# Kernel tuning notes

Measured on AMD Instinct MI355X. Metric: run time of the kernel, lower is better.

The kernel has to match this reference:

```python
import jax, jax.numpy as jnp
import numpy as np

B, U, D = 128, 200, 512

def setup_inputs() -> dict:
    key = jax.random.key(0)
    k1, k2, k3 = jax.random.split(key, 3)
    input_real = jax.random.normal(k1, (B, D, D), dtype=jnp.float32)
    input_imag = jax.random.normal(k2, (B, D, D), dtype=jnp.float32)
    # keras 'uniform' initializer: U(-0.05, 0.05); unit_norm constraint normalizes over axes (1,2)
    kernel = jax.random.uniform(k3, (U, D, 2), dtype=jnp.float32, minval=-0.05, maxval=0.05)
    kernel = kernel / jnp.linalg.norm(kernel.reshape(U, -1), axis=1)[:, None, None]
    return {"input_real": input_real, "input_imag": input_imag, "kernel": kernel}

def reference(input_real, input_imag, kernel):
    # kernel: [U, D, 2] -> real/imag measurement vectors
    kr = kernel[:, :, 0]  # [U, D]
    ki = kernel[:, :, 1]  # [U, D]
    # Original: M_real = kr kr^T - ki ki^T ; M_imag = ki kr^T + kr ki^T (outer products per unit)
    # out[b,n] = trace(R_b @ M_real_n) - trace(I_b @ M_imag_n)
    # trace(A @ (u v^T)) = sum_ij A[i,j] u[j] v[i] -> quadratic form, avoids [B,U,D,D] tiles.
    t_real = (jnp.einsum('bij,nj,ni->bn', input_real, kr, kr)
              - jnp.einsum('bij,nj,ni->bn', input_real, ki, ki))
    t_imag = (jnp.einsum('bij,nj,ni->bn', input_imag, ki, kr)
              + jnp.einsum('bij,nj,ni->bn', input_imag, kr, ki))
    return t_real - t_imag  # [B, U]
```

## Files before the change

kernel.cpp:

```cpp
#include <hip/hip_runtime.h>
#include <hip/hip_bf16.h>

#define BB 128
#define UU 200
#define DD 512
#define NPAD 256
#define ASTR 40
#define WSTR 40

typedef __attribute__((ext_vector_type(8))) short short8;
typedef __attribute__((ext_vector_type(4))) float f32x4;

__device__ __forceinline__ unsigned short f2bf(float x) {
    union { float f; unsigned u; } v; v.f = x;
    unsigned r = v.u + 0x7FFFu + ((v.u >> 16) & 1u);
    return (unsigned short)(r >> 16);
}

__global__ void zero_out_kernel(float* __restrict__ out) {
    int i = blockIdx.x * 256 + threadIdx.x;
    if (i < BB * UU) out[i] = 0.0f;
}

__global__ __launch_bounds__(512, 4) void cm_gemm_kernel(
    const float* __restrict__ Ar, const float* __restrict__ Ai,
    const float* __restrict__ Kt, float* __restrict__ out)
{
    __shared__ short sAr[BB * ASTR];
    __shared__ short sAi[BB * ASTR];
    __shared__ short sWr[NPAD * WSTR];
    __shared__ short sWi[NPAD * WSTR];

    const int tid  = threadIdx.x;
    const int irow = blockIdx.x;
    const int w    = tid >> 6;
    const int lane = tid & 63;
    const int mw   = (w & 1) * 64;
    const int nw   = (w >> 1) * 64;
    const int rrow = lane & 15;
    const int quad = lane >> 4;

    const int nW = tid >> 1;
    const int jh = (tid & 1) * 16;
    float krI = 0.0f, kiI = 0.0f;
    if (nW < UU) {
        const float2* k2 = (const float2*)Kt;
        float2 s = k2[(size_t)nW * DD + irow];
        krI = s.x; kiI = s.y;
    }

    const int brow0 = tid >> 3;
    const int grp   = tid & 7;
    const size_t aoff0 = (size_t)brow0 * DD * DD + (size_t)irow * DD + (size_t)grp * 4;
    const size_t aoff1 = aoff0 + (size_t)64 * DD * DD;

    f32x4 acc[4][4];
#pragma unroll
    for (int a = 0; a < 4; ++a)
#pragma unroll
        for (int b = 0; b < 4; ++b) acc[a][b] = (f32x4)(0.0f);

    for (int jw = 0; jw < DD; jw += 32) {
        f32x4 vr0 = *(const f32x4*)(Ar + aoff0 + jw);
        f32x4 vr1 = *(const f32x4*)(Ar + aoff1 + jw);
        f32x4 vi0 = *(const f32x4*)(Ai + aoff0 + jw);
        f32x4 vi1 = *(const f32x4*)(Ai + aoff1 + jw);

        {
            union { unsigned short s[4]; uint2 u; } t0, t1, t2, t3;
#pragma unroll
            for (int q = 0; q < 4; ++q) {
                t0.s[q] = f2bf(vr0[q]); t1.s[q] = f2bf(vr1[q]);
                t2.s[q] = f2bf(vi0[q]); t3.s[q] = f2bf(vi1[q]);
            }
            *(uint2*)&sAr[ brow0       * ASTR + grp * 4] = t0.u;
            *(uint2*)&sAr[(brow0 + 64) * ASTR + grp * 4] = t1.u;
            *(uint2*)&sAi[ brow0       * ASTR + grp * 4] = t2.u;
            *(uint2*)&sAi[(brow0 + 64) * ASTR + grp * 4] = t3.u;
        }

        if (nW < UU) {
            const f32x4* kv = (const f32x4*)(Kt + (size_t)nW * DD * 2 + (size_t)(jw + jh) * 2);
#pragma unroll
            for (int q = 0; q < 8; ++q) {
                f32x4 v = kv[q];
                float wr0 =  krI * v[0] - kiI * v[1];
                float wi0 = -(krI * v[1] + kiI * v[0]);
                float wr1 =  krI * v[2] - kiI * v[3];
                float wi1 = -(krI * v[3] + kiI * v[2]);
                unsigned pr = (unsigned)f2bf(wr0) | ((unsigned)f2bf(wr1) << 16);
                unsigned pi = (unsigned)f2bf(wi0) | ((unsigned)f2bf(wi1) << 16);
                *(unsigned*)&sWr[nW * WSTR + jh + 2 * q] = pr;
                *(unsigned*)&sWi[nW * WSTR + jh + 2 * q] = pi;
            }
        } else {
#pragma unroll
            for (int q = 0; q < 8; ++q) {
                *(unsigned*)&sWr[nW * WSTR + jh + 2 * q] = 0u;
                *(unsigned*)&sWi[nW * WSTR + jh + 2 * q] = 0u;
            }
        }

        __syncthreads();

#pragma unroll
        for (int ph = 0; ph < 2; ++ph) {
            const short* sA = ph ? sAi : sAr;
            const short* sW = ph ? sWi : sWr;
            short8 af[4], bf[4];
#pragma unroll
            for (int t = 0; t < 4; ++t) {
                af[t] = *(const short8*)&sA[(mw + t * 16 + rrow) * ASTR + quad * 8];
                bf[t] = *(const short8*)&sW[(nw + t * 16 + rrow) * WSTR + quad * 8];
            }
#pragma unroll
            for (int ti = 0; ti < 4; ++ti)
#pragma unroll
                for (int tj = 0; tj < 4; ++tj)
                    acc[ti][tj] = __builtin_amdgcn_mfma_f32_16x16x32_bf16(
                        af[ti], bf[tj], acc[ti][tj], 0, 0, 0);
        }

        __syncthreads();
    }

#pragma unroll
    for (int ti = 0; ti < 4; ++ti) {
        int m = mw + ti * 16 + quad * 4;
#pragma unroll
        for (int tj = 0; tj < 4; ++tj) {
            int n = nw + tj * 16 + rrow;
            if (n < UU) {
#pragma unroll
                for (int r = 0; r < 4; ++r)
                    atomicAdd(&out[(size_t)(m + r) * UU + n], acc[ti][tj][r]);
            }
        }
    }
}

extern "C" void kernel_launch(void* const* d_in, const int* in_sizes, int n_in,
                              void* d_out, int out_size, void* d_ws, size_t ws_size,
                              hipStream_t stream) {
    const float* Ar = (const float*)d_in[0];
    const float* Ai = (const float*)d_in[1];
    const float* Kt = (const float*)d_in[2];
    float* out = (float*)d_out;

    hipLaunchKernelGGL(zero_out_kernel, dim3((BB * UU + 255) / 256), dim3(256), 0, stream, out);
    hipLaunchKernelGGL(cm_gemm_kernel, dim3(DD), dim3(512), 0, stream, Ar, Ai, Kt, out);
}
```

Measured before the change: 375.3 us.

## Prefetch next A tile into registers and replace atomics with workspace reduction

The A loads for the next k-step are now issued before the MFMA phase, a register-level software prefetch meant to hide global load latency. When enough workspace is available, each of the 512 blocks writes its partial [B,U] result to its own workspace slice with plain stores. A separate reduce kernel then sums the slices in 8 groups and finishes with fewer atomics. This removes heavy contention from 512-way atomicAdd on the same outputs. The cost is about 52 MB of extra workspace writes and reads plus an added launch.

```diff
diff --git a/kernel.cpp b/kernel.cpp
--- a/kernel.cpp
+++ b/kernel.cpp
@@ -7,6 +7,7 @@
 #define NPAD 256
 #define ASTR 40
 #define WSTR 40
+#define NSPLIT 512
 
 typedef __attribute__((ext_vector_type(8))) short short8;
 typedef __attribute__((ext_vector_type(4))) float f32x4;
@@ -22,9 +23,21 @@
     if (i < BB * UU) out[i] = 0.0f;
 }
 
+__global__ void reduce_kernel(const float* __restrict__ ws, float* __restrict__ out) {
+    int o = blockIdx.x * 256 + threadIdx.x;
+    if (o >= BB * UU) return;
+    int p0 = blockIdx.y * (NSPLIT / 8);
+    float s = 0.0f;
+#pragma unroll 8
+    for (int p = 0; p < NSPLIT / 8; ++p)
+        s += ws[(size_t)(p0 + p) * (BB * UU) + o];
+    atomicAdd(&out[o], s);
+}
+
+template<bool USE_WS>
 __global__ __launch_bounds__(512, 4) void cm_gemm_kernel(
     const float* __restrict__ Ar, const float* __restrict__ Ai,
-    const float* __restrict__ Kt, float* __restrict__ out)
+    const float* __restrict__ Kt, float* __restrict__ dst)
 {
     __shared__ short sAr[BB * ASTR];
     __shared__ short sAi[BB * ASTR];
@@ -60,11 +73,13 @@
 #pragma unroll
         for (int b = 0; b < 4; ++b) acc[a][b] = (f32x4)(0.0f);
 
-    for (int jw = 0; jw < DD; jw += 32) {
-        f32x4 vr0 = *(const f32x4*)(Ar + aoff0 + jw);
-        f32x4 vr1 = *(const f32x4*)(Ar + aoff1 + jw);
-        f32x4 vi0 = *(const f32x4*)(Ai + aoff0 + jw);
-        f32x4 vi1 = *(const f32x4*)(Ai + aoff1 + jw);
+    f32x4 vr0 = *(const f32x4*)(Ar + aoff0);
+    f32x4 vr1 = *(const f32x4*)(Ar + aoff1);
+    f32x4 vi0 = *(const f32x4*)(Ai + aoff0);
+    f32x4 vi1 = *(const f32x4*)(Ai + aoff1);
+
+    for (int it = 0; it < 16; ++it) {
+        const int jw = it * 32;
 
         {
             union { unsigned short s[4]; uint2 u; } t0, t1, t2, t3;
@@ -103,6 +118,12 @@
 
         __syncthreads();
 
+        const int jn = (it < 15) ? (jw + 32) : 0;
+        f32x4 nr0 = *(const f32x4*)(Ar + aoff0 + jn);
+        f32x4 nr1 = *(const f32x4*)(Ar + aoff1 + jn);
+        f32x4 ni0 = *(const f32x4*)(Ai + aoff0 + jn);
+        f32x4 ni1 = *(const f32x4*)(Ai + aoff1 + jn);
+
 #pragma unroll
         for (int ph = 0; ph < 2; ++ph) {
             const short* sA = ph ? sAi : sAr;
@@ -122,18 +143,37 @@
         }
 
         __syncthreads();
-    }
-
-#pragma unroll
-    for (int ti = 0; ti < 4; ++ti) {
-        int m = mw + ti * 16 + quad * 4;
-#pragma unroll
-        for (int tj = 0; tj < 4; ++tj) {
-            int n = nw + tj * 16 + rrow;
-            if (n < UU) {
-#pragma unroll
-                for (int r = 0; r < 4; ++r)
-                    atomicAdd(&out[(size_t)(m + r) * UU + n], acc[ti][tj][r]);
+
+        vr0 = nr0; vr1 = nr1; vi0 = ni0; vi1 = ni1;
+    }
+
+    if (USE_WS) {
+        float* wsp = dst + (size_t)irow * (BB * UU);
+#pragma unroll
+        for (int ti = 0; ti < 4; ++ti) {
+            int m = mw + ti * 16 + quad * 4;
+#pragma unroll
+            for (int tj = 0; tj < 4; ++tj) {
+                int n = nw + tj * 16 + rrow;
+                if (n < UU) {
+#pragma unroll
+                    for (int r = 0; r < 4; ++r)
+                        wsp[(size_t)(m + r) * UU + n] = acc[ti][tj][r];
+                }
+            }
+        }
+    } else {
+#pragma unroll
+        for (int ti = 0; ti < 4; ++ti) {
+            int m = mw + ti * 16 + quad * 4;
+#pragma unroll
+            for (int tj = 0; tj < 4; ++tj) {
+                int n = nw + tj * 16 + rrow;
+                if (n < UU) {
+#pragma unroll
+                    for (int r = 0; r < 4; ++r)
+                        atomicAdd(&dst[(size_t)(m + r) * UU + n], acc[ti][tj][r]);
+                }
             }
         }
     }
@@ -147,6 +187,18 @@
     const float* Kt = (const float*)d_in[2];
     float* out = (float*)d_out;
 
-    hipLaunchKernelGGL(zero_out_kernel, dim3((BB * UU + 255) / 256), dim3(256), 0, stream, out);
-    hipLaunchKernelGGL(cm_gemm_kernel, dim3(DD), dim3(512), 0, stream, Ar, Ai, Kt, out);
-}
+    const size_t ws_need = (size_t)NSPLIT * BB * UU * sizeof(float);
+
+    if (ws_size >= ws_need) {
+        float* ws = (float*)d_ws;
+        hipLaunchKernelGGL((cm_gemm_kernel<true>), dim3(NSPLIT), dim3(512), 0, stream,
+                           Ar, Ai, Kt, ws);
+        hipLaunchKernelGGL(zero_out_kernel, dim3((BB * UU + 255) / 256), dim3(256), 0, stream, out);
+        hipLaunchKernelGGL(reduce_kernel, dim3((BB * UU + 255) / 256, 8), dim3(256), 0, stream,
+                           ws, out);
+    } else {
+        hipLaunchKernelGGL(zero_out_kernel, dim3((BB * UU + 255) / 256), dim3(256), 0, stream, out);
+        hipLaunchKernelGGL((cm_gemm_kernel<false>), dim3(NSPLIT), dim3(512), 0, stream,
+                           Ar, Ai, Kt, out);
+    }
+}
```

New measurement: 322.2 us. 14.2% less time.

## Restructure complex GEMM with 1024-thread blocks, bf16 kernel prepack, and workspace reduction

Applied to the files above, without the earlier changes.

Adds a pre-pass that packs the kernel into bf16 pairs. The main GEMM now uses 1024-thread blocks where each wave owns 16 output units and builds its B fragments in registers from the packed kernel, reusing the imaginary fragments across phases. The A tile is staged in swizzled, double-buffered 128x128 shared memory with register prefetch of the next tile. Most per-row partials go to a workspace and are summed by a separate reduce kernel instead of global atomics. This targets redundant W construction in LDS, LDS bank conflicts and atomic contention, at the cost of extra launches, a large workspace and a fallback path if the workspace is too small.

```diff
diff --git a/kernel.cpp b/kernel.cpp
--- a/kernel.cpp
+++ b/kernel.cpp
@@ -1,15 +1,20 @@
 #include <hip/hip_runtime.h>
 #include <hip/hip_bf16.h>
+#include <string.h>
 
 #define BB 128
 #define UU 200
 #define DD 512
-#define NPAD 256
-#define ASTR 40
-#define WSTR 40
+#define NP 256
+#define NWS 504
 
 typedef __attribute__((ext_vector_type(8))) short short8;
 typedef __attribute__((ext_vector_type(4))) float f32x4;
+
+__device__ __forceinline__ unsigned pack_bf16_2(float a, float b) {
+    __hip_bfloat162 h = __float22bfloat162_rn(make_float2(a, b));
+    unsigned u; memcpy(&u, &h, 4); return u;
+}
 
 __device__ __forceinline__ unsigned short f2bf(float x) {
     union { float f; unsigned u; } v; v.f = x;
@@ -17,81 +22,221 @@
     return (unsigned short)(r >> 16);
 }
 
+__global__ void kb_build_kernel(const float* __restrict__ Kt, unsigned* __restrict__ Kb) {
+    int idx = blockIdx.x * 256 + threadIdx.x;
+    int n = idx >> 9, j = idx & 511;
+    unsigned v = 0u;
+    if (n < UU) {
+        float2 s = ((const float2*)Kt)[(size_t)n * DD + j];
+        v = pack_bf16_2(s.x, s.y);
+    }
+    Kb[idx] = v;
+}
+
 __global__ void zero_out_kernel(float* __restrict__ out) {
     int i = blockIdx.x * 256 + threadIdx.x;
     if (i < BB * UU) out[i] = 0.0f;
 }
 
-__global__ __launch_bounds__(512, 4) void cm_gemm_kernel(
+__global__ void reduce_kernel(const float* __restrict__ ws, float* __restrict__ out) {
+    int o = blockIdx.x * 256 + threadIdx.x;
+    if (o >= BB * UU) return;
+    int p0 = blockIdx.y * 36;
+    float s = 0.0f;
+#pragma unroll
+    for (int p = 0; p < 36; ++p)
+        s += ws[(size_t)(p0 + p) * (BB * UU) + o];
+    atomicAdd(&out[o], s);
+}
+
+__global__ __launch_bounds__(1024, 4) void cm_gemm2_kernel(
     const float* __restrict__ Ar, const float* __restrict__ Ai,
-    const float* __restrict__ Kt, float* __restrict__ out)
+    const float* __restrict__ Kt, const unsigned* __restrict__ Kb,
+    float* __restrict__ ws, float* __restrict__ out)
 {
-    __shared__ short sAr[BB * ASTR];
-    __shared__ short sAi[BB * ASTR];
-    __shared__ short sWr[NPAD * WSTR];
-    __shared__ short sWi[NPAD * WSTR];
+    __shared__ short sA[2 * 128 * 128];
 
     const int tid  = threadIdx.x;
     const int irow = blockIdx.x;
     const int w    = tid >> 6;
     const int lane = tid & 63;
-    const int mw   = (w & 1) * 64;
-    const int nw   = (w >> 1) * 64;
     const int rrow = lane & 15;
     const int quad = lane >> 4;
-
-    const int nW = tid >> 1;
-    const int jh = (tid & 1) * 16;
-    float krI = 0.0f, kiI = 0.0f;
-    if (nW < UU) {
-        const float2* k2 = (const float2*)Kt;
-        float2 s = k2[(size_t)nW * DD + irow];
+    const int nn   = w * 16 + rrow;
+    const int xr   = rrow & 7;
+
+    float krI = 0.f, kiI = 0.f;
+    if (nn < UU) {
+        float2 s = ((const float2*)Kt)[(size_t)nn * DD + irow];
         krI = s.x; kiI = s.y;
     }
-
-    const int brow0 = tid >> 3;
-    const int grp   = tid & 7;
+    const float nkrI = -krI, nkiI = -kiI;
+
+    const int g = tid & 31, r0 = tid >> 5;
+    unsigned boff[4];
+    int waddr[4];
+#pragma unroll
+    for (int l = 0; l < 4; ++l) {
+        int row = r0 + 32 * l;
+        boff[l] = (unsigned)row * (DD * DD) + (unsigned)irow * DD + g * 4;
+        waddr[l] = row * 128 + (((g >> 1) ^ (row & 7)) * 8) + (g & 1) * 4;
+    }
+
+    f32x4 acc[8];
+#pragma unroll
+    for (int t = 0; t < 8; ++t) acc[t] = (f32x4)(0.f);
+
+    f32x4 pf[4];
+#pragma unroll
+    for (int l = 0; l < 4; ++l) pf[l] = *(const f32x4*)(Ar + boff[l]);
+
+    short8 bi_sv[4];
+
+    for (int t = 0; t < 8; ++t) {
+        const int ph = t & 1;
+        const int j0 = (t >> 1) * 128;
+        short* sb = &sA[(t & 1) * (128 * 128)];
+
+#pragma unroll
+        for (int l = 0; l < 4; ++l) {
+            uint2 u;
+            u.x = pack_bf16_2(pf[l][0], pf[l][1]);
+            u.y = pack_bf16_2(pf[l][2], pf[l][3]);
+            *(uint2*)&sb[waddr[l]] = u;
+        }
+        __syncthreads();
+
+        if (t < 7) {
+            const int tn = t + 1;
+            const float* P = (tn & 1) ? Ai : Ar;
+            const unsigned jn = (unsigned)((tn >> 1) * 128);
+#pragma unroll
+            for (int l = 0; l < 4; ++l) pf[l] = *(const f32x4*)(P + boff[l] + jn);
+        }
+
+        const unsigned* kbp = Kb + (unsigned)nn * DD + j0 + quad * 8;
+        uint4 nx0, nx1;
+        if (ph == 0) { nx0 = *(const uint4*)kbp; nx1 = *(const uint4*)(kbp + 4); }
+
+#pragma unroll
+        for (int kk = 0; kk < 4; ++kk) {
+            short8 bfrag;
+            if (ph == 0) {
+                uint4 c0 = nx0, c1 = nx1;
+                if (kk < 3) {
+                    nx0 = *(const uint4*)(kbp + (kk + 1) * 32);
+                    nx1 = *(const uint4*)(kbp + (kk + 1) * 32 + 4);
+                }
+                unsigned dw[8] = {c0.x, c0.y, c0.z, c0.w, c1.x, c1.y, c1.z, c1.w};
+                float wr[8], wi[8];
+#pragma unroll
+                for (int e = 0; e < 8; ++e) {
+                    union { unsigned u; float f; } a, b;
+                    a.u = dw[e] << 16;
+                    b.u = dw[e] & 0xFFFF0000u;
+                    wr[e] = krI * a.f + nkiI * b.f;
+                    wi[e] = nkrI * b.f + nkiI * a.f;
+                }
+                union { short8 v; unsigned u[4]; } pr, pi;
+#pragma unroll
+                for (int e = 0; e < 4; ++e) {
+                    pr.u[e] = pack_bf16_2(wr[2 * e], wr[2 * e + 1]);
+                    pi.u[e] = pack_bf16_2(wi[2 * e], wi[2 * e + 1]);
+                }
+                bfrag = pr.v;
+                bi_sv[kk] = pi.v;
+            } else {
+                bfrag = bi_sv[kk];
+            }
+
+#pragma unroll
+            for (int h = 0; h < 2; ++h) {
+                short8 af[4];
+#pragma unroll
+                for (int q = 0; q < 4; ++q) {
+                    int row = (h * 4 + q) * 16 + rrow;
+                    int gran = (kk * 4 + quad) ^ xr;
+                    af[q] = *(const short8*)&sb[row * 128 + gran * 8];
+                }
+#pragma unroll
+                for (int q = 0; q < 4; ++q)
+                    acc[h * 4 + q] = __builtin_amdgcn_mfma_f32_16x16x32_bf16(
+                        af[q], bfrag, acc[h * 4 + q], 0, 0, 0);
+            }
+        }
+    }
+
+    if (nn < UU) {
+        if (irow < NWS) {
+            float* wsp = ws + (size_t)irow * (BB * UU);
+#pragma unroll
+            for (int ti = 0; ti < 8; ++ti) {
+                int m = ti * 16 + quad * 4;
+#pragma unroll
+                for (int r = 0; r < 4; ++r)
+                    wsp[(size_t)(m + r) * UU + nn] = acc[ti][r];
+            }
+        } else {
+#pragma unroll
+            for (int ti = 0; ti < 8; ++ti) {
+                int m = ti * 16 + quad * 4;
+#pragma unroll
+                for (int r = 0; r < 4; ++r)
+                    atomicAdd(&out[(size_t)(m + r) * UU + nn], acc[ti][r]);
+            }
+        }
+    }
+}
+
+#define ASTR 40
+#define WSTR 40
+__global__ __launch_bounds__(512, 4) void cm_gemm_fb_kernel(
+    const float* __restrict__ Ar, const float* __restrict__ Ai,
+    const float* __restrict__ Kt, float* __restrict__ dst)
+{
+    __shared__ short sAr[BB * ASTR];
+    __shared__ short sAi[BB * ASTR];
+    __shared__ short sWr[NP * WSTR];
+    __shared__ short sWi[NP * WSTR];
+    const int tid = threadIdx.x, irow = blockIdx.x;
+    const int w = tid >> 6, lane = tid & 63;
+    const int mw = (w & 1) * 64, nw = (w >> 1) * 64;
+    const int rrow = lane & 15, quad = lane >> 4;
+    const int nW = tid >> 1, jh = (tid & 1) * 16;
+    float krI = 0.f, kiI = 0.f;
+    if (nW < UU) { float2 s = ((const float2*)Kt)[(size_t)nW * DD + irow]; krI = s.x; kiI = s.y; }
+    const int brow0 = tid >> 3, grp = tid & 7;
     const size_t aoff0 = (size_t)brow0 * DD * DD + (size_t)irow * DD + (size_t)grp * 4;
     const size_t aoff1 = aoff0 + (size_t)64 * DD * DD;
-
     f32x4 acc[4][4];
 #pragma unroll
     for (int a = 0; a < 4; ++a)
 #pragma unroll
-        for (int b = 0; b < 4; ++b) acc[a][b] = (f32x4)(0.0f);
-
+        for (int b = 0; b < 4; ++b) acc[a][b] = (f32x4)(0.f);
     for (int jw = 0; jw < DD; jw += 32) {
         f32x4 vr0 = *(const f32x4*)(Ar + aoff0 + jw);
         f32x4 vr1 = *(const f32x4*)(Ar + aoff1 + jw);
         f32x4 vi0 = *(const f32x4*)(Ai + aoff0 + jw);
         f32x4 vi1 = *(const f32x4*)(Ai + aoff1 + jw);
-
-        {
-            union { unsigned short s[4]; uint2 u; } t0, t1, t2, t3;
-#pragma unroll
-            for (int q = 0; q < 4; ++q) {
-                t0.s[q] = f2bf(vr0[q]); t1.s[q] = f2bf(vr1[q]);
-                t2.s[q] = f2bf(vi0[q]); t3.s[q] = f2bf(vi1[q]);
-            }
-            *(uint2*)&sAr[ brow0       * ASTR + grp * 4] = t0.u;
-            *(uint2*)&sAr[(brow0 + 64) * ASTR + grp * 4] = t1.u;
-            *(uint2*)&sAi[ brow0       * ASTR + grp * 4] = t2.u;
-            *(uint2*)&sAi[(brow0 + 64) * ASTR + grp * 4] = t3.u;
-        }
-
+        union { unsigned short s[4]; uint2 u; } t0, t1, t2, t3;
+#pragma unroll
+        for (int q = 0; q < 4; ++q) {
+            t0.s[q] = f2bf(vr0[q]); t1.s[q] = f2bf(vr1[q]);
+            t2.s[q] = f2bf(vi0[q]); t3.s[q] = f2bf(vi1[q]);
+        }
+        *(uint2*)&sAr[ brow0       * ASTR + grp * 4] = t0.u;
+        *(uint2*)&sAr[(brow0 + 64) * ASTR + grp * 4] = t1.u;
+        *(uint2*)&sAi[ brow0       * ASTR + grp * 4] = t2.u;
+        *(uint2*)&sAi[(brow0 + 64) * ASTR + grp * 4] = t3.u;
         if (nW < UU) {
             const f32x4* kv = (const f32x4*)(Kt + (size_t)nW * DD * 2 + (size_t)(jw + jh) * 2);
 #pragma unroll
             for (int q = 0; q < 8; ++q) {
                 f32x4 v = kv[q];
-                float wr0 =  krI * v[0] - kiI * v[1];
-                float wi0 = -(krI * v[1] + kiI * v[0]);
-                float wr1 =  krI * v[2] - kiI * v[3];
-                float wi1 = -(krI * v[3] + kiI * v[2]);
-                unsigned pr = (unsigned)f2bf(wr0) | ((unsigned)f2bf(wr1) << 16);
-                unsigned pi = (unsigned)f2bf(wi0) | ((unsigned)f2bf(wi1) << 16);
-                *(unsigned*)&sWr[nW * WSTR + jh + 2 * q] = pr;
-                *(unsigned*)&sWi[nW * WSTR + jh + 2 * q] = pi;
+                float wr0 = krI * v[0] - kiI * v[1], wi0 = -(krI * v[1] + kiI * v[0]);
+                float wr1 = krI * v[2] - kiI * v[3], wi1 = -(krI * v[3] + kiI * v[2]);
+                *(unsigned*)&sWr[nW * WSTR + jh + 2 * q] = (unsigned)f2bf(wr0) | ((unsigned)f2bf(wr1) << 16);
+                *(unsigned*)&sWi[nW * WSTR + jh + 2 * q] = (unsigned)f2bf(wi0) | ((unsigned)f2bf(wi1) << 16);
             }
         } else {
 #pragma unroll
@@ -100,9 +245,7 @@
                 *(unsigned*)&sWi[nW * WSTR + jh + 2 * q] = 0u;
             }
         }
-
         __syncthreads();
-
 #pragma unroll
         for (int ph = 0; ph < 2; ++ph) {
             const short* sA = ph ? sAi : sAr;
@@ -117,24 +260,20 @@
             for (int ti = 0; ti < 4; ++ti)
 #pragma unroll
                 for (int tj = 0; tj < 4; ++tj)
-                    acc[ti][tj] = __builtin_amdgcn_mfma_f32_16x16x32_bf16(
-                        af[ti], bf[tj], acc[ti][tj], 0, 0, 0);
-        }
-
+                    acc[ti][tj] = __builtin_amdgcn_mfma_f32_16x16x32_bf16(af[ti], bf[tj], acc[ti][tj], 0, 0, 0);
+        }
         __syncthreads();
     }
-
 #pragma unroll
     for (int ti = 0; ti < 4; ++ti) {
         int m = mw + ti * 16 + quad * 4;
 #pragma unroll
         for (int tj = 0; tj < 4; ++tj) {
             int n = nw + tj * 16 + rrow;
-            if (n < UU) {
+            if (n < UU)
 #pragma unroll
                 for (int r = 0; r < 4; ++r)
-                    atomicAdd(&out[(size_t)(m + r) * UU + n], acc[ti][tj][r]);
-            }
+                    atomicAdd(&dst[(size_t)(m + r) * UU + n], acc[ti][tj][r]);
         }
     }
 }
@@ -147,6 +286,19 @@
     const float* Kt = (const float*)d_in[2];
     float* out = (float*)d_out;
 
-    hipLaunchKernelGGL(zero_out_kernel, dim3((BB * UU + 255) / 256), dim3(256), 0, stream, out);
-    hipLaunchKernelGGL(cm_gemm_kernel, dim3(DD), dim3(512), 0, stream, Ar, Ai, Kt, out);
-}
+    const size_t kb_dwords = (size_t)NP * DD;
+    const size_t ws_need = kb_dwords * 4 + (size_t)NWS * BB * UU * 4;
+
+    if (ws_size >= ws_need) {
+        unsigned* Kb = (unsigned*)d_ws;
+        float* ws = (float*)d_ws + kb_dwords;
+        hipLaunchKernelGGL(kb_build_kernel, dim3(512), dim3(256), 0, stream, Kt, Kb);
+        hipLaunchKernelGGL(zero_out_kernel, dim3(100), dim3(256), 0, stream, out);
+        hipLaunchKernelGGL(cm_gemm2_kernel, dim3(DD), dim3(1024), 0, stream,
+                           Ar, Ai, Kt, Kb, ws, out);
+        hipLaunchKernelGGL(reduce_kernel, dim3(100, 14), dim3(256), 0, stream, ws, out);
+    } else {
+        hipLaunchKernelGGL(zero_out_kernel, dim3(100), dim3(256), 0, stream, out);
+        hipLaunchKernelGGL(cm_gemm_fb_kernel, dim3(DD), dim3(512), 0, stream, Ar, Ai, Kt, out);
+    }
+}
```

Measured after the change: 306.3 us. -18.4%, faster.
